# Kernel optimization log

Hardware: AMD Instinct MI355X
Metric: run time of the kernel (lower is better)

Reference implementation:

```python
import jax, jax.numpy as jnp
import numpy as np

EPS = 1e-5
HEADS = 8


def _bn(x, p):
    # p: [4, C] rows = (gamma, beta, running_mean, running_var); channel axis = 1 (eval-mode BN)
    shape = (1, p.shape[1]) + (1,) * (x.ndim - 2)
    g = p[0].reshape(shape); b = p[1].reshape(shape)
    m = p[2].reshape(shape); v = p[3].reshape(shape)
    return (x - m) * (g / jnp.sqrt(v + EPS)) + b


def _conv1x1(x, w):
    # x: [N, Cin, H, W], w: [Cout, Cin]
    return jnp.einsum('oc,nchw->nohw', w, x)


def _axial(x, kqv_w, kqv_bn, logits_bn, rel_enc, ks, height_dim):
    # x: [B, C, H, W]
    if height_dim:
        x = jnp.transpose(x, (0, 3, 1, 2))  # [B, W, C, H] -> attend over H (=ks)
    else:
        x = jnp.transpose(x, (0, 2, 1, 3))  # [B, H, C, W] -> attend over W (=ks)
    b, w, d, h = x.shape
    dh = d // HEADS
    xf = x.reshape(b * w, d, h)
    kqv = jnp.einsum('oc,ncl->nol', kqv_w, xf)          # conv1d k=1, [n, 2d, h]
    kqv = _bn(kqv, kqv_bn)
    kqv = kqv.reshape(b * w, HEADS, dh * 2, h)
    k = kqv[:, :, : dh // 2]                            # [n, H, dh/2, h]
    q = kqv[:, :, dh // 2: dh]                          # [n, H, dh/2, h]
    v = kqv[:, :, dh:]                                  # [n, H, dh,   h]
    # relative position encodings
    idx = jnp.arange(ks)[None, :] - jnp.arange(ks)[:, None] + ks - 1  # [ks, ks]
    rel = rel_enc[:, idx.reshape(-1)].reshape(dh * 2, ks, ks)
    q_enc = rel[: dh // 2]
    k_enc = rel[dh // 2: dh]
    v_enc = rel[dh:]
    qk = jnp.einsum('nhdx,nhdy->nhxy', q, k)
    qr = jnp.einsum('nhdx,dxy->nhxy', q, q_enc)
    kr = jnp.einsum('nhdx,dxy->nhyx', k, k_enc)         # einsum + transpose(2,3)
    logits = jnp.concatenate([qk, qr, kr], axis=1)       # [n, 3*H, h, h]
    logits = _bn(logits, logits_bn)
    logits = logits.reshape(b * w, 3, HEADS, h, h).sum(axis=1)
    weights = jax.nn.softmax(logits, axis=3)             # [n, H, h, h]
    attn = jnp.einsum('nhxy,nhdy->nhdx', weights, v)
    attn_enc = jnp.einsum('nhxy,dxy->nhdx', weights, v_enc)
    # cat along last dim + reshape + sum(dim=-2) in torch == elementwise sum here
    out = (attn + attn_enc).reshape(b, w, d, h)
    if height_dim:
        out = jnp.transpose(out, (0, 2, 3, 1))  # [B, C, H, W]
    else:
        out = jnp.transpose(out, (0, 2, 1, 3))  # [B, C, H, W]
    return out


def setup_inputs() -> dict:
    key = jax.random.key(0)
    ks = jax.random.split(key, 13)
    def rn(k, shape, s=0.05):
        return jax.random.normal(k, shape, jnp.float32) * s
    def rp(k, shape):
        return jax.random.uniform(k, shape, jnp.float32, minval=0.1, maxval=1.0)
    return {
        'x': jax.random.normal(ks[0], (1, 64, 256, 128), jnp.float32),
        'conv1_w': rn(ks[1], (64, 64)),
        'bn1': rp(ks[2], (4, 64)),
        'kqv_w_h': rn(ks[3], (128, 64)),
        'kqv_bn_h': rp(ks[4], (4, 128)),
        'logits_bn_h': rp(ks[5], (4, 24)),
        'rel_enc_h': rn(ks[6], (16, 511)),
        'kqv_w_w': rn(ks[7], (128, 64)),
        'kqv_bn_w': rp(ks[8], (4, 128)),
        'logits_bn_w': rp(ks[9], (4, 24)),
        'rel_enc_w': rn(ks[10], (16, 255)),
        'conv3_w': rn(ks[11], (64, 64)),
        'bn3': rp(ks[12], (4, 64)),
    }


def reference(x, conv1_w, bn1, kqv_w_h, kqv_bn_h, logits_bn_h, rel_enc_h,
              kqv_w_w, kqv_bn_w, logits_bn_w, rel_enc_w, conv3_w, bn3):
    out = jax.nn.relu(_bn(_conv1x1(x, conv1_w), bn1))
    out = _axial(out, kqv_w_h, kqv_bn_h, logits_bn_h, rel_enc_h, 256, True)
    out = _axial(out, kqv_w_w, kqv_bn_w, logits_bn_w, rel_enc_w, 128, False)
    out = jax.nn.relu(out)
    out = _bn(_conv1x1(out, conv3_w), bn3)
    return jax.nn.relu(out + x)
```

## Files before the change

kernel.cpp:

```cpp
#include <hip/hip_runtime.h>
#include <stdint.h>

#define EPSF 1e-5f
#define LOG2E 1.4426950408889634f

__device__ __forceinline__ float bflo(uint32_t u){ union{uint32_t u;float f;}c; c.u=u<<16; return c.f; }
__device__ __forceinline__ float bfhi(uint32_t u){ union{uint32_t u;float f;}c; c.u=u&0xffff0000u; return c.f; }
__device__ __forceinline__ float bfhiraw(uint32_t u){ union{uint32_t u;float f;}c; c.u=u; return c.f; }
__device__ __forceinline__ uint32_t f2bf(float f){ union{float f;uint32_t u;}c; c.f=f; uint32_t u=c.u; return (u + 0x7fffu + ((u>>16)&1u)) >> 16; }
__device__ __forceinline__ uint32_t pk2(float a, float b){ return f2bf(a) | (f2bf(b)<<16); }

__global__ void k_relpack(const float* __restrict__ rel, uint4* __restrict__ rqk,
                          uint4* __restrict__ rve, int NJ) {
  int j = threadIdx.x;
  if (j >= NJ) return;
  const float* q = rel;
  const float* k = rel + 4*NJ;
  const float* v = rel + 8*NJ;
  int jr = NJ-1-j;
  uint4 a;
  a.x = pk2(q[0*NJ+j], q[1*NJ+j]);
  a.y = pk2(q[2*NJ+j], q[3*NJ+j]);
  a.z = pk2(k[0*NJ+jr], k[1*NJ+jr]);
  a.w = pk2(k[2*NJ+jr], k[3*NJ+jr]);
  rqk[j] = a;
  uint4 b;
  b.x = pk2(v[0*NJ+j], v[1*NJ+j]);
  b.y = pk2(v[2*NJ+j], v[3*NJ+j]);
  b.z = pk2(v[4*NJ+j], v[5*NJ+j]);
  b.w = pk2(v[6*NJ+j], v[7*NJ+j]);
  rve[j] = b;
}

template<bool IN_NHWC, bool RESID>
__global__ __launch_bounds__(256)
void k_conv(const float* __restrict__ in, const float* __restrict__ w,
            const float* __restrict__ bn, const float* __restrict__ resid,
            float* __restrict__ out) {
  int p = blockIdx.x * 256 + threadIdx.x;
  int ob = blockIdx.y * 16;
  float xv[64];
  if (IN_NHWC) {
    const float4* src = (const float4*)(in + (size_t)p*64);
    #pragma unroll
    for (int c4 = 0; c4 < 16; ++c4) {
      float4 t = src[c4];
      xv[4*c4+0]=t.x; xv[4*c4+1]=t.y; xv[4*c4+2]=t.z; xv[4*c4+3]=t.w;
    }
  } else {
    #pragma unroll
    for (int c = 0; c < 64; ++c) xv[c] = in[c*32768 + p];
  }
  #pragma unroll
  for (int r = 0; r < 16; ++r) {
    int o = ob + r;
    const float* wr = w + o*64;
    float acc = 0.f;
    #pragma unroll
    for (int c = 0; c < 64; ++c) acc = fmaf(wr[c], xv[c], acc);
    float s = bn[o] * rsqrtf(bn[192+o] + EPSF);
    float val = fmaf(acc, s, fmaf(-bn[128+o], s, bn[64+o]));
    if (RESID) {
      val = fmaxf(val + resid[o*32768 + p], 0.f);
      out[o*32768 + p] = val;
    } else {
      out[(size_t)p*64 + o] = fmaxf(val, 0.f);
    }
  }
}

template<int LEN, int RS, int CS>
__global__ __launch_bounds__(256)
void k_kqv(const float* __restrict__ in, const float* __restrict__ w,
           const float* __restrict__ bn, uint4* __restrict__ kvV,
           uint2* __restrict__ kvK, float* __restrict__ qb) {
  int n = blockIdx.x;
  int head = __builtin_amdgcn_readfirstlane(blockIdx.y*4 + (threadIdx.x>>6));
  int lane = threadIdx.x & 63;
  int y = blockIdx.z*64 + lane;
  const float* src = in + ((size_t)y*RS + (size_t)n*CS)*64;
  float xv[64];
  #pragma unroll
  for (int c4 = 0; c4 < 16; ++c4) {
    float4 t = ((const float4*)src)[c4];
    xv[4*c4+0]=t.x; xv[4*c4+1]=t.y; xv[4*c4+2]=t.z; xv[4*c4+3]=t.w;
  }
  float val[16];
  #pragma unroll
  for (int r = 0; r < 16; ++r) {
    int o = head*16 + r;
    const float* wr = w + o*64;
    float acc = 0.f;
    #pragma unroll
    for (int c = 0; c < 64; ++c) acc = fmaf(wr[c], xv[c], acc);
    float s = bn[o] * rsqrtf(bn[384+o] + EPSF);
    val[r] = fmaf(acc, s, fmaf(-bn[256+o], s, bn[128+o]));
  }
  size_t base = ((size_t)n*8 + head)*LEN + y;
  uint4 vv; vv.x = pk2(val[8],val[9]);  vv.y = pk2(val[10],val[11]);
            vv.z = pk2(val[12],val[13]); vv.w = pk2(val[14],val[15]);
  kvV[base] = vv;
  uint2 kk; kk.x = pk2(val[0],val[1]); kk.y = pk2(val[2],val[3]);
  kvK[base] = kk;
  float4 qq; qq.x = val[4]; qq.y = val[5]; qq.z = val[6]; qq.w = val[7];
  *(float4*)(qb + base*4) = qq;
}

template<int LEN, bool RELUO, int XS, int NS>
__global__ __launch_bounds__(LEN, 2)
void k_attn2(const uint4* __restrict__ kvV, const uint2* __restrict__ kvK,
             const float* __restrict__ qb, const uint4* __restrict__ rqk,
             const uint4* __restrict__ rve, const float* __restrict__ lbn,
             float* __restrict__ out) {
  constexpr int NJ = 2*LEN-1;
  constexpr int HALF = LEN/2;
  constexpr int CH = 4;
  int n  = blockIdx.x >> 3;
  int hd = blockIdx.x & 7;
  int t  = threadIdx.x;

  __shared__ __align__(16) char pool[(size_t)LEN*48 + (size_t)NJ*48];
  float4* sK   = (float4*)(pool);
  float4* sVa  = (float4*)(pool + (size_t)LEN*16);
  float4* sVb  = (float4*)(pool + (size_t)LEN*32);
  uint4*  sT   = (uint4*) (pool + (size_t)LEN*48);
  float4* sVE0 = (float4*)(pool + (size_t)LEN*48 + (size_t)NJ*16);
  float4* sVE1 = (float4*)(pool + (size_t)LEN*48 + (size_t)NJ*32);

  size_t kvbase = ((size_t)n*8 + hd)*LEN;
  {
    uint2 kk = kvK[kvbase + t];
    uint4 vv = kvV[kvbase + t];
    sK[t]  = make_float4(bflo(kk.x), bfhi(kk.x), bflo(kk.y), bfhi(kk.y));
    sVa[t] = make_float4(bflo(vv.x), bfhi(vv.x), bflo(vv.y), bfhi(vv.y));
    sVb[t] = make_float4(bflo(vv.z), bfhi(vv.z), bflo(vv.w), bfhi(vv.w));
  }
  for (int j = t; j < NJ; j += LEN) {
    sT[j] = rqk[j];
    uint4 ve = rve[j];
    sVE0[j] = make_float4(bflo(ve.x), bfhi(ve.x), bflo(ve.y), bfhi(ve.y));
    sVE1[j] = make_float4(bflo(ve.z), bfhi(ve.z), bflo(ve.w), bfhi(ve.w));
  }

  float A0,A1,A2,Bc;
  {
    int c0 = hd, c1 = 8+hd, c2 = 16+hd;
    float s0 = lbn[c0]*rsqrtf(lbn[72+c0]+EPSF);
    float s1 = lbn[c1]*rsqrtf(lbn[72+c1]+EPSF);
    float s2 = lbn[c2]*rsqrtf(lbn[72+c2]+EPSF);
    float t0 = fmaf(-lbn[48+c0], s0, lbn[24+c0]);
    float t1 = fmaf(-lbn[48+c1], s1, lbn[24+c1]);
    float t2 = fmaf(-lbn[48+c2], s2, lbn[24+c2]);
    A0 = s0*LOG2E; A1 = s1*LOG2E; A2 = s2*LOG2E; Bc = (t0+t1+t2)*LOG2E;
  }

  int g  = t / HALF;
  int tl = t % HALF;
  int y0 = g * HALF;

  float q[2][4];
  #pragma unroll
  for (int i = 0; i < 2; ++i) {
    float4 qq = *(const float4*)(qb + (kvbase + tl + i*HALF)*4);
    q[i][0]=qq.x; q[i][1]=qq.y; q[i][2]=qq.z; q[i][3]=qq.w;
  }
  float m[2], ss[2], acc[2][8], lr[2][CH];
  #pragma unroll
  for (int i=0;i<2;++i){ m[i]=-3.0e38f; ss[i]=0.f;
    #pragma unroll
    for(int d=0;d<8;++d) acc[i][d]=0.f; }

  __syncthreads();

  for (int yc = 0; yc < HALF; yc += CH) {
    #pragma unroll
    for (int c = 0; c < CH; ++c) {
      int y = y0 + yc + c;
      float4 kk = sK[y];
      #pragma unroll
      for (int i = 0; i < 2; ++i) {
        int j = y - (tl + i*HALF) + (LEN-1);
        uint4 qe = sT[j];
        float qk = fmaf(q[i][3],kk.w, fmaf(q[i][2],kk.z, fmaf(q[i][1],kk.y, q[i][0]*kk.x)));
        float qr = fmaf(q[i][1],bfhiraw(qe.x), q[i][0]*bflo(qe.x));
        qr = fmaf(q[i][3],bfhiraw(qe.y), fmaf(q[i][2],bflo(qe.y), qr));
        float kr = fmaf(kk.y,bfhiraw(qe.z), kk.x*bflo(qe.z));
        kr = fmaf(kk.w,bfhiraw(qe.w), fmaf(kk.z,bflo(qe.w), kr));
        lr[i][c] = fmaf(qk,A0, fmaf(qr,A1, fmaf(kr,A2, Bc)));
      }
    }
    #pragma unroll
    for (int i = 0; i < 2; ++i) {
      float cm = fmaxf(fmaxf(lr[i][0], lr[i][1]), fmaxf(lr[i][2], lr[i][3]));
      float mn = fmaxf(m[i], cm);
      float sc = __builtin_amdgcn_exp2f(m[i] - mn);
      m[i] = mn; ss[i] *= sc;
      #pragma unroll
      for (int d = 0; d < 8; ++d) acc[i][d] *= sc;
    }
    #pragma unroll
    for (int c = 0; c < CH; ++c) {
      int y = y0 + yc + c;
      float4 va = sVa[y], vb = sVb[y];
      #pragma unroll
      for (int i = 0; i < 2; ++i) {
        int j = y - (tl + i*HALF) + (LEN-1);
        float4 ea = sVE0[j];
        float4 eb = sVE1[j];
        float e = __builtin_amdgcn_exp2f(lr[i][c] - m[i]);
        ss[i] += e;
        acc[i][0] = fmaf(e, va.x + ea.x, acc[i][0]);
        acc[i][1] = fmaf(e, va.y + ea.y, acc[i][1]);
        acc[i][2] = fmaf(e, va.z + ea.z, acc[i][2]);
        acc[i][3] = fmaf(e, va.w + ea.w, acc[i][3]);
        acc[i][4] = fmaf(e, vb.x + eb.x, acc[i][4]);
        acc[i][5] = fmaf(e, vb.y + eb.y, acc[i][5]);
        acc[i][6] = fmaf(e, vb.z + eb.z, acc[i][6]);
        acc[i][7] = fmaf(e, vb.w + eb.w, acc[i][7]);
      }
    }
  }

  __syncthreads();
  float4* M0 = (float4*)(pool);
  float4* M1 = (float4*)(pool + (size_t)HALF*32);
  float2* MS = (float2*)(pool + (size_t)HALF*64);
  if (g == 1) {
    #pragma unroll
    for (int i = 0; i < 2; ++i) {
      M0[tl*2+i] = make_float4(acc[i][0],acc[i][1],acc[i][2],acc[i][3]);
      M1[tl*2+i] = make_float4(acc[i][4],acc[i][5],acc[i][6],acc[i][7]);
      MS[tl*2+i] = make_float2(m[i], ss[i]);
    }
  }
  __syncthreads();
  if (g == 0) {
    #pragma unroll
    for (int i = 0; i < 2; ++i) {
      float2 os = MS[tl*2+i];
      float4 a0 = M0[tl*2+i];
      float4 a1 = M1[tl*2+i];
      float M  = fmaxf(m[i], os.x);
      float w0 = __builtin_amdgcn_exp2f(m[i] - M);
      float w1 = __builtin_amdgcn_exp2f(os.x - M);
      float inv = 1.0f / (ss[i]*w0 + os.y*w1);
      int x = tl + i*HALF;
      float* dst = out + ((size_t)x*XS + (size_t)n*NS)*64 + hd*8;
      float4 lo, hi;
      lo.x = (acc[i][0]*w0 + a0.x*w1)*inv;
      lo.y = (acc[i][1]*w0 + a0.y*w1)*inv;
      lo.z = (acc[i][2]*w0 + a0.z*w1)*inv;
      lo.w = (acc[i][3]*w0 + a0.w*w1)*inv;
      hi.x = (acc[i][4]*w0 + a1.x*w1)*inv;
      hi.y = (acc[i][5]*w0 + a1.y*w1)*inv;
      hi.z = (acc[i][6]*w0 + a1.z*w1)*inv;
      hi.w = (acc[i][7]*w0 + a1.w*w1)*inv;
      if (RELUO) {
        lo.x=fmaxf(lo.x,0.f); lo.y=fmaxf(lo.y,0.f); lo.z=fmaxf(lo.z,0.f); lo.w=fmaxf(lo.w,0.f);
        hi.x=fmaxf(hi.x,0.f); hi.y=fmaxf(hi.y,0.f); hi.z=fmaxf(hi.z,0.f); hi.w=fmaxf(hi.w,0.f);
      }
      *(float4*)dst = lo;
      *((float4*)dst + 1) = hi;
    }
  }
}

extern "C" void kernel_launch(void* const* d_in, const int* in_sizes, int n_in,
                              void* d_out, int out_size, void* d_ws, size_t ws_size,
                              hipStream_t stream) {
  const float* x         = (const float*)d_in[0];
  const float* conv1_w   = (const float*)d_in[1];
  const float* bn1       = (const float*)d_in[2];
  const float* kqv_w_h   = (const float*)d_in[3];
  const float* kqv_bn_h  = (const float*)d_in[4];
  const float* lbn_h     = (const float*)d_in[5];
  const float* rel_h     = (const float*)d_in[6];
  const float* kqv_w_w   = (const float*)d_in[7];
  const float* kqv_bn_w  = (const float*)d_in[8];
  const float* lbn_w     = (const float*)d_in[9];
  const float* rel_w     = (const float*)d_in[10];
  const float* conv3_w   = (const float*)d_in[11];
  const float* bn3       = (const float*)d_in[12];
  float* outp = (float*)d_out;
  char* ws = (char*)d_ws;

  float* A    = (float*)(ws);
  uint4* kvV  = (uint4*)(ws + 8388608);
  uint2* kvK  = (uint2*)(ws + 12582912);
  float* qb   = (float*)(ws + 14680064);
  uint4* rqkH = (uint4*)(ws + 18874368);
  uint4* rveH = (uint4*)(ws + 18882560);
  uint4* rqkW = (uint4*)(ws + 18890752);
  uint4* rveW = (uint4*)(ws + 18894848);

  k_relpack<<<1, 512, 0, stream>>>(rel_h, rqkH, rveH, 511);
  k_relpack<<<1, 256, 0, stream>>>(rel_w, rqkW, rveW, 255);

  k_conv<false,false><<<dim3(128,4), 256, 0, stream>>>(x, conv1_w, bn1, nullptr, A);

  k_kqv<256,128,1><<<dim3(128,2,4), 256, 0, stream>>>(A, kqv_w_h, kqv_bn_h, kvV, kvK, qb);
  k_attn2<256,false,128,1><<<1024, 256, 0, stream>>>(kvV, kvK, qb, rqkH, rveH, lbn_h, A);

  k_kqv<128,1,128><<<dim3(256,2,2), 256, 0, stream>>>(A, kqv_w_w, kqv_bn_w, kvV, kvK, qb);
  k_attn2<128,true,1,128><<<2048, 128, 0, stream>>>(kvV, kvK, qb, rqkW, rveW, lbn_w, A);

  k_conv<true,true><<<dim3(128,4), 256, 0, stream>>>(A, conv3_w, bn3, x, outp);
}
```

Baseline: 208.3 us.

## Switch attention operands to packed fp16 with dot2, stage conv/kqv through LDS

Replaces bf16 storage with packed fp16 and computes the logits with v_dot2 (fdot2) and packed half adds for V plus the positional encoding. Q is also stored as fp16, and LDS holds the packed form, which halves the shared memory footprint. conv1, conv3 and kqv now transpose through an LDS tile for coalesced loads and stores, kqv runs 512-thread blocks that share one input tile across all 8 heads, and the two relpack launches are merged into one. fp16 gives more mantissa than bf16 but less range, and the half-precision adds could lose some accuracy.

Result: slower. 251.5 us (+20.7%).

```diff
diff --git a/kernel.cpp b/kernel.cpp
--- a/kernel.cpp
+++ b/kernel.cpp
@@ -4,14 +4,32 @@
 #define EPSF 1e-5f
 #define LOG2E 1.4426950408889634f
 
-__device__ __forceinline__ float bflo(uint32_t u){ union{uint32_t u;float f;}c; c.u=u<<16; return c.f; }
-__device__ __forceinline__ float bfhi(uint32_t u){ union{uint32_t u;float f;}c; c.u=u&0xffff0000u; return c.f; }
-__device__ __forceinline__ float bfhiraw(uint32_t u){ union{uint32_t u;float f;}c; c.u=u; return c.f; }
-__device__ __forceinline__ uint32_t f2bf(float f){ union{float f;uint32_t u;}c; c.f=f; uint32_t u=c.u; return (u + 0x7fffu + ((u>>16)&1u)) >> 16; }
-__device__ __forceinline__ uint32_t pk2(float a, float b){ return f2bf(a) | (f2bf(b)<<16); }
-
-__global__ void k_relpack(const float* __restrict__ rel, uint4* __restrict__ rqk,
-                          uint4* __restrict__ rve, int NJ) {
+typedef _Float16 h2 __attribute__((ext_vector_type(2)));
+union UH2 { uint32_t u; h2 h; };
+
+__device__ __forceinline__ uint32_t pkh(float a, float b){
+  UH2 c; c.h.x = (_Float16)a; c.h.y = (_Float16)b; return c.u;
+}
+__device__ __forceinline__ h2 ash2(uint32_t u){ UH2 c; c.u = u; return c.h; }
+
+#if __has_builtin(__builtin_amdgcn_fdot2)
+__device__ __forceinline__ float fdot2u(uint32_t a, uint32_t b, float c){
+  return __builtin_amdgcn_fdot2(ash2(a), ash2(b), c, false);
+}
+#else
+__device__ __forceinline__ float fdot2u(uint32_t a, uint32_t b, float c){
+  h2 x = ash2(a), y = ash2(b);
+  return fmaf((float)x.y, (float)y.y, fmaf((float)x.x, (float)y.x, c));
+}
+#endif
+
+__global__ void k_relpack(const float* __restrict__ relH, const float* __restrict__ relW,
+                          uint4* __restrict__ rqkH, uint4* __restrict__ rveH,
+                          uint4* __restrict__ rqkW, uint4* __restrict__ rveW) {
+  int NJ = blockIdx.x ? 255 : 511;
+  const float* rel = blockIdx.x ? relW : relH;
+  uint4* rqk = blockIdx.x ? rqkW : rqkH;
+  uint4* rve = blockIdx.x ? rveW : rveH;
   int j = threadIdx.x;
   if (j >= NJ) return;
   const float* q = rel;
@@ -19,76 +37,85 @@
   const float* v = rel + 8*NJ;
   int jr = NJ-1-j;
   uint4 a;
-  a.x = pk2(q[0*NJ+j], q[1*NJ+j]);
-  a.y = pk2(q[2*NJ+j], q[3*NJ+j]);
-  a.z = pk2(k[0*NJ+jr], k[1*NJ+jr]);
-  a.w = pk2(k[2*NJ+jr], k[3*NJ+jr]);
+  a.x = pkh(q[0*NJ+j], q[1*NJ+j]);
+  a.y = pkh(q[2*NJ+j], q[3*NJ+j]);
+  a.z = pkh(k[0*NJ+jr], k[1*NJ+jr]);
+  a.w = pkh(k[2*NJ+jr], k[3*NJ+jr]);
   rqk[j] = a;
   uint4 b;
-  b.x = pk2(v[0*NJ+j], v[1*NJ+j]);
-  b.y = pk2(v[2*NJ+j], v[3*NJ+j]);
-  b.z = pk2(v[4*NJ+j], v[5*NJ+j]);
-  b.w = pk2(v[6*NJ+j], v[7*NJ+j]);
+  b.x = pkh(v[0*NJ+j], v[1*NJ+j]);
+  b.y = pkh(v[2*NJ+j], v[3*NJ+j]);
+  b.z = pkh(v[4*NJ+j], v[5*NJ+j]);
+  b.w = pkh(v[6*NJ+j], v[7*NJ+j]);
   rve[j] = b;
 }
 
-template<bool IN_NHWC, bool RESID>
 __global__ __launch_bounds__(256)
-void k_conv(const float* __restrict__ in, const float* __restrict__ w,
-            const float* __restrict__ bn, const float* __restrict__ resid,
-            float* __restrict__ out) {
-  int p = blockIdx.x * 256 + threadIdx.x;
-  int ob = blockIdx.y * 16;
+void k_conv1(const float* __restrict__ in, const float* __restrict__ w,
+             const float* __restrict__ bn, float* __restrict__ out) {
+  __shared__ float L[64*65];
+  int tid = threadIdx.x;
+  int p0 = blockIdx.x * 64;
+  int lane = tid & 63, wv = tid >> 6;
+  #pragma unroll
+  for (int rr = 0; rr < 16; ++rr) {
+    int c = wv*16 + rr;
+    L[c*64 + lane] = in[(size_t)c*32768 + p0 + lane];
+  }
+  __syncthreads();
   float xv[64];
-  if (IN_NHWC) {
-    const float4* src = (const float4*)(in + (size_t)p*64);
-    #pragma unroll
-    for (int c4 = 0; c4 < 16; ++c4) {
-      float4 t = src[c4];
-      xv[4*c4+0]=t.x; xv[4*c4+1]=t.y; xv[4*c4+2]=t.z; xv[4*c4+3]=t.w;
-    }
-  } else {
-    #pragma unroll
-    for (int c = 0; c < 64; ++c) xv[c] = in[c*32768 + p];
-  }
+  #pragma unroll
+  for (int c = 0; c < 64; ++c) xv[c] = L[c*64 + lane];
+  float val[16];
   #pragma unroll
   for (int r = 0; r < 16; ++r) {
-    int o = ob + r;
+    int o = wv*16 + r;
     const float* wr = w + o*64;
     float acc = 0.f;
     #pragma unroll
     for (int c = 0; c < 64; ++c) acc = fmaf(wr[c], xv[c], acc);
     float s = bn[o] * rsqrtf(bn[192+o] + EPSF);
-    float val = fmaf(acc, s, fmaf(-bn[128+o], s, bn[64+o]));
-    if (RESID) {
-      val = fmaxf(val + resid[o*32768 + p], 0.f);
-      out[o*32768 + p] = val;
-    } else {
-      out[(size_t)p*64 + o] = fmaxf(val, 0.f);
-    }
+    val[r] = fmaxf(fmaf(acc, s, fmaf(-bn[128+o], s, bn[64+o])), 0.f);
+  }
+  __syncthreads();
+  #pragma unroll
+  for (int r = 0; r < 16; ++r) L[lane*65 + wv*16 + r] = val[r];
+  __syncthreads();
+  float4* dst = (float4*)(out + (size_t)p0*64);
+  #pragma unroll
+  for (int k = 0; k < 4; ++k) {
+    int f4 = tid + k*256;
+    int f = f4*4; int p = f >> 6, o = f & 63;
+    float4 v;
+    v.x = L[p*65+o]; v.y = L[p*65+o+1]; v.z = L[p*65+o+2]; v.w = L[p*65+o+3];
+    dst[f4] = v;
   }
 }
 
 template<int LEN, int RS, int CS>
-__global__ __launch_bounds__(256)
+__global__ __launch_bounds__(512)
 void k_kqv(const float* __restrict__ in, const float* __restrict__ w,
            const float* __restrict__ bn, uint4* __restrict__ kvV,
-           uint2* __restrict__ kvK, float* __restrict__ qb) {
+           uint2* __restrict__ kvK, uint2* __restrict__ qb) {
+  __shared__ float L[64*65];
+  int tid = threadIdx.x;
   int n = blockIdx.x;
-  int head = __builtin_amdgcn_readfirstlane(blockIdx.y*4 + (threadIdx.x>>6));
-  int lane = threadIdx.x & 63;
-  int y = blockIdx.z*64 + lane;
-  const float* src = in + ((size_t)y*RS + (size_t)n*CS)*64;
+  int y0 = blockIdx.y * 64;
+  #pragma unroll
+  for (int rr = 0; rr < 8; ++rr) {
+    int idx = tid + rr*512;
+    int yy = idx >> 6, c = idx & 63;
+    L[yy*65 + c] = in[((size_t)(y0+yy)*RS + (size_t)n*CS)*64 + c];
+  }
+  __syncthreads();
+  int hd = tid >> 6, yy = tid & 63;
   float xv[64];
   #pragma unroll
-  for (int c4 = 0; c4 < 16; ++c4) {
-    float4 t = ((const float4*)src)[c4];
-    xv[4*c4+0]=t.x; xv[4*c4+1]=t.y; xv[4*c4+2]=t.z; xv[4*c4+3]=t.w;
-  }
+  for (int c = 0; c < 64; ++c) xv[c] = L[yy*65 + c];
   float val[16];
   #pragma unroll
   for (int r = 0; r < 16; ++r) {
-    int o = head*16 + r;
+    int o = hd*16 + r;
     const float* wr = w + o*64;
     float acc = 0.f;
     #pragma unroll
@@ -96,20 +123,17 @@
     float s = bn[o] * rsqrtf(bn[384+o] + EPSF);
     val[r] = fmaf(acc, s, fmaf(-bn[256+o], s, bn[128+o]));
   }
-  size_t base = ((size_t)n*8 + head)*LEN + y;
-  uint4 vv; vv.x = pk2(val[8],val[9]);  vv.y = pk2(val[10],val[11]);
-            vv.z = pk2(val[12],val[13]); vv.w = pk2(val[14],val[15]);
-  kvV[base] = vv;
-  uint2 kk; kk.x = pk2(val[0],val[1]); kk.y = pk2(val[2],val[3]);
-  kvK[base] = kk;
-  float4 qq; qq.x = val[4]; qq.y = val[5]; qq.z = val[6]; qq.w = val[7];
-  *(float4*)(qb + base*4) = qq;
+  size_t base = ((size_t)n*8 + hd)*LEN + (y0 + yy);
+  kvK[base] = make_uint2(pkh(val[0],val[1]), pkh(val[2],val[3]));
+  qb[base]  = make_uint2(pkh(val[4],val[5]), pkh(val[6],val[7]));
+  kvV[base] = make_uint4(pkh(val[8],val[9]),  pkh(val[10],val[11]),
+                         pkh(val[12],val[13]), pkh(val[14],val[15]));
 }
 
 template<int LEN, bool RELUO, int XS, int NS>
 __global__ __launch_bounds__(LEN, 2)
-void k_attn2(const uint4* __restrict__ kvV, const uint2* __restrict__ kvK,
-             const float* __restrict__ qb, const uint4* __restrict__ rqk,
+void k_attn3(const uint4* __restrict__ kvV, const uint2* __restrict__ kvK,
+             const uint2* __restrict__ qb, const uint4* __restrict__ rqk,
              const uint4* __restrict__ rve, const float* __restrict__ lbn,
              float* __restrict__ out) {
   constexpr int NJ = 2*LEN-1;
@@ -119,28 +143,16 @@
   int hd = blockIdx.x & 7;
   int t  = threadIdx.x;
 
-  __shared__ __align__(16) char pool[(size_t)LEN*48 + (size_t)NJ*48];
-  float4* sK   = (float4*)(pool);
-  float4* sVa  = (float4*)(pool + (size_t)LEN*16);
-  float4* sVb  = (float4*)(pool + (size_t)LEN*32);
-  uint4*  sT   = (uint4*) (pool + (size_t)LEN*48);
-  float4* sVE0 = (float4*)(pool + (size_t)LEN*48 + (size_t)NJ*16);
-  float4* sVE1 = (float4*)(pool + (size_t)LEN*48 + (size_t)NJ*32);
+  __shared__ __align__(16) char pool[(size_t)LEN*24 + (size_t)NJ*32];
+  uint2* sK  = (uint2*)(pool);
+  uint4* sV  = (uint4*)(pool + (size_t)LEN*8);
+  uint4* sT  = (uint4*)(pool + (size_t)LEN*24);
+  uint4* sVE = (uint4*)(pool + (size_t)LEN*24 + (size_t)NJ*16);
 
   size_t kvbase = ((size_t)n*8 + hd)*LEN;
-  {
-    uint2 kk = kvK[kvbase + t];
-    uint4 vv = kvV[kvbase + t];
-    sK[t]  = make_float4(bflo(kk.x), bfhi(kk.x), bflo(kk.y), bfhi(kk.y));
-    sVa[t] = make_float4(bflo(vv.x), bfhi(vv.x), bflo(vv.y), bfhi(vv.y));
-    sVb[t] = make_float4(bflo(vv.z), bfhi(vv.z), bflo(vv.w), bfhi(vv.w));
-  }
-  for (int j = t; j < NJ; j += LEN) {
-    sT[j] = rqk[j];
-    uint4 ve = rve[j];
-    sVE0[j] = make_float4(bflo(ve.x), bfhi(ve.x), bflo(ve.y), bfhi(ve.y));
-    sVE1[j] = make_float4(bflo(ve.z), bfhi(ve.z), bflo(ve.w), bfhi(ve.w));
-  }
+  sK[t] = kvK[kvbase + t];
+  sV[t] = kvV[kvbase + t];
+  for (int j = t; j < NJ; j += LEN) { sT[j] = rqk[j]; sVE[j] = rve[j]; }
 
   float A0,A1,A2,Bc;
   {
@@ -158,12 +170,10 @@
   int tl = t % HALF;
   int y0 = g * HALF;
 
-  float q[2][4];
-  #pragma unroll
-  for (int i = 0; i < 2; ++i) {
-    float4 qq = *(const float4*)(qb + (kvbase + tl + i*HALF)*4);
-    q[i][0]=qq.x; q[i][1]=qq.y; q[i][2]=qq.z; q[i][3]=qq.w;
-  }
+  uint2 q[2];
+  q[0] = qb[kvbase + tl];
+  q[1] = qb[kvbase + tl + HALF];
+
   float m[2], ss[2], acc[2][8], lr[2][CH];
   #pragma unroll
   for (int i=0;i<2;++i){ m[i]=-3.0e38f; ss[i]=0.f;
@@ -176,16 +186,14 @@
     #pragma unroll
     for (int c = 0; c < CH; ++c) {
       int y = y0 + yc + c;
-      float4 kk = sK[y];
+      uint2 kk = sK[y];
       #pragma unroll
       for (int i = 0; i < 2; ++i) {
         int j = y - (tl + i*HALF) + (LEN-1);
         uint4 qe = sT[j];
-        float qk = fmaf(q[i][3],kk.w, fmaf(q[i][2],kk.z, fmaf(q[i][1],kk.y, q[i][0]*kk.x)));
-        float qr = fmaf(q[i][1],bfhiraw(qe.x), q[i][0]*bflo(qe.x));
-        qr = fmaf(q[i][3],bfhiraw(qe.y), fmaf(q[i][2],bflo(qe.y), qr));
-        float kr = fmaf(kk.y,bfhiraw(qe.z), kk.x*bflo(qe.z));
-        kr = fmaf(kk.w,bfhiraw(qe.w), fmaf(kk.z,bflo(qe.w), kr));
+        float qk = fdot2u(q[i].x, kk.x, fdot2u(q[i].y, kk.y, 0.f));
+        float qr = fdot2u(q[i].x, qe.x, fdot2u(q[i].y, qe.y, 0.f));
+        float kr = fdot2u(kk.x, qe.z, fdot2u(kk.y, qe.w, 0.f));
         lr[i][c] = fmaf(qk,A0, fmaf(qr,A1, fmaf(kr,A2, Bc)));
       }
     }
@@ -201,22 +209,25 @@
     #pragma unroll
     for (int c = 0; c < CH; ++c) {
       int y = y0 + yc + c;
-      float4 va = sVa[y], vb = sVb[y];
+      uint4 vv = sV[y];
       #pragma unroll
       for (int i = 0; i < 2; ++i) {
         int j = y - (tl + i*HALF) + (LEN-1);
-        float4 ea = sVE0[j];
-        float4 eb = sVE1[j];
+        uint4 ve = sVE[j];
         float e = __builtin_amdgcn_exp2f(lr[i][c] - m[i]);
         ss[i] += e;
-        acc[i][0] = fmaf(e, va.x + ea.x, acc[i][0]);
-        acc[i][1] = fmaf(e, va.y + ea.y, acc[i][1]);
-        acc[i][2] = fmaf(e, va.z + ea.z, acc[i][2]);
-        acc[i][3] = fmaf(e, va.w + ea.w, acc[i][3]);
-        acc[i][4] = fmaf(e, vb.x + eb.x, acc[i][4]);
-        acc[i][5] = fmaf(e, vb.y + eb.y, acc[i][5]);
-        acc[i][6] = fmaf(e, vb.z + eb.z, acc[i][6]);
-        acc[i][7] = fmaf(e, vb.w + eb.w, acc[i][7]);
+        h2 s0 = ash2(vv.x) + ash2(ve.x);
+        h2 s1 = ash2(vv.y) + ash2(ve.y);
+        h2 s2 = ash2(vv.z) + ash2(ve.z);
+        h2 s3 = ash2(vv.w) + ash2(ve.w);
+        acc[i][0] = fmaf(e, (float)s0.x, acc[i][0]);
+        acc[i][1] = fmaf(e, (float)s0.y, acc[i][1]);
+        acc[i][2] = fmaf(e, (float)s1.x, acc[i][2]);
+        acc[i][3] = fmaf(e, (float)s1.y, acc[i][3]);
+        acc[i][4] = fmaf(e, (float)s2.x, acc[i][4]);
+        acc[i][5] = fmaf(e, (float)s2.y, acc[i][5]);
+        acc[i][6] = fmaf(e, (float)s3.x, acc[i][6]);
+        acc[i][7] = fmaf(e, (float)s3.y, acc[i][7]);
       }
     }
   }
@@ -265,6 +276,40 @@
   }
 }
 
+__global__ __launch_bounds__(256)
+void k_conv3(const float* __restrict__ in, const float* __restrict__ w,
+             const float* __restrict__ bn, const float* __restrict__ resid,
+             float* __restrict__ out) {
+  __shared__ float L[64*65];
+  int tid = threadIdx.x;
+  int p0 = blockIdx.x * 64;
+  const float4* src = (const float4*)(in + (size_t)p0*64);
+  #pragma unroll
+  for (int k = 0; k < 4; ++k) {
+    int f4 = tid + k*256;
+    float4 v = src[f4];
+    int f = f4*4; int p = f >> 6, o = f & 63;
+    L[p*65+o] = v.x; L[p*65+o+1] = v.y; L[p*65+o+2] = v.z; L[p*65+o+3] = v.w;
+  }
+  __syncthreads();
+  int lane = tid & 63, wv = tid >> 6;
+  float xv[64];
+  #pragma unroll
+  for (int c = 0; c < 64; ++c) xv[c] = L[lane*65 + c];
+  #pragma unroll
+  for (int r = 0; r < 16; ++r) {
+    int o = wv*16 + r;
+    const float* wr = w + o*64;
+    float acc = 0.f;
+    #pragma unroll
+    for (int c = 0; c < 64; ++c) acc = fmaf(wr[c], xv[c], acc);
+    float s = bn[o] * rsqrtf(bn[192+o] + EPSF);
+    float val = fmaf(acc, s, fmaf(-bn[128+o], s, bn[64+o]));
+    size_t idx = (size_t)o*32768 + p0 + lane;
+    out[idx] = fmaxf(val + resid[idx], 0.f);
+  }
+}
+
 extern "C" void kernel_launch(void* const* d_in, const int* in_sizes, int n_in,
                               void* d_out, int out_size, void* d_ws, size_t ws_size,
                               hipStream_t stream) {
@@ -287,22 +332,21 @@
   float* A    = (float*)(ws);
   uint4* kvV  = (uint4*)(ws + 8388608);
   uint2* kvK  = (uint2*)(ws + 12582912);
-  float* qb   = (float*)(ws + 14680064);
+  uint2* qb   = (uint2*)(ws + 14680064);
   uint4* rqkH = (uint4*)(ws + 18874368);
   uint4* rveH = (uint4*)(ws + 18882560);
   uint4* rqkW = (uint4*)(ws + 18890752);
   uint4* rveW = (uint4*)(ws + 18894848);
 
-  k_relpack<<<1, 512, 0, stream>>>(rel_h, rqkH, rveH, 511);
-  k_relpack<<<1, 256, 0, stream>>>(rel_w, rqkW, rveW, 255);
-
-  k_conv<false,false><<<dim3(128,4), 256, 0, stream>>>(x, conv1_w, bn1, nullptr, A);
-
-  k_kqv<256,128,1><<<dim3(128,2,4), 256, 0, stream>>>(A, kqv_w_h, kqv_bn_h, kvV, kvK, qb);
-  k_attn2<256,false,128,1><<<1024, 256, 0, stream>>>(kvV, kvK, qb, rqkH, rveH, lbn_h, A);
-
-  k_kqv<128,1,128><<<dim3(256,2,2), 256, 0, stream>>>(A, kqv_w_w, kqv_bn_w, kvV, kvK, qb);
-  k_attn2<128,true,1,128><<<2048, 128, 0, stream>>>(kvV, kvK, qb, rqkW, rveW, lbn_w, A);
-
-  k_conv<true,true><<<dim3(128,4), 256, 0, stream>>>(A, conv3_w, bn3, x, outp);
-}
+  k_relpack<<<2, 512, 0, stream>>>(rel_h, rel_w, rqkH, rveH, rqkW, rveW);
+
+  k_conv1<<<512, 256, 0, stream>>>(x, conv1_w, bn1, A);
+
+  k_kqv<256,128,1><<<dim3(128,4), 512, 0, stream>>>(A, kqv_w_h, kqv_bn_h, kvV, kvK, qb);
+  k_attn3<256,false,128,1><<<1024, 256, 0, stream>>>(kvV, kvK, qb, rqkH, rveH, lbn_h, A);
+
+  k_kqv<128,1,128><<<dim3(256,2), 512, 0, stream>>>(A, kqv_w_w, kqv_bn_w, kvV, kvK, qb);
+  k_attn3<128,true,1,128><<<2048, 128, 0, stream>>>(kvV, kvK, qb, rqkW, rveW, lbn_w, A);
+
+  k_conv3<<<512, 256, 0, stream>>>(A, conv3_w, bn3, x, outp);
+}
```
